# Kernel tuning notes

Measured on AMD Instinct MI355X. Metric: run time of the kernel, lower is better.

The kernel has to match this reference:

```python
import jax, jax.numpy as jnp
from jax import lax
import numpy as np

LENY = 1048576
NRBF = 11
A_PRIME = 1.0
B_PRIME = 1.0 / 60.0


def safe_sigmoid(x):
    return jax.nn.sigmoid(jnp.clip(x, -10.0, 10.0))


def setup_inputs() -> dict:
    key = jax.random.key(0)
    k = jax.random.split(key, 6)
    return {
        "yin": jax.random.normal(k[0], (LENY, 2), dtype=jnp.float32),
        "xstar_a": jax.random.normal(k[1], (LENY, 2), dtype=jnp.float32),
        "xstar_b": jax.random.normal(k[2], (LENY, 2), dtype=jnp.float32),
        "rbfw_raw": jax.random.normal(k[3], (1,), dtype=jnp.float32),
        "weights": jax.random.normal(k[4], (NRBF, 1), dtype=jnp.float32),
        "gain1_raw": jax.random.normal(k[5], (1,), dtype=jnp.float32),
        "gain2_raw": jax.random.normal(jax.random.fold_in(key, 7), (1,), dtype=jnp.float32),
    }


def reference(yin, xstar_a, xstar_b, rbfw_raw, weights, gain1_raw, gain2_raw):
    leny = yin.shape[0]
    # normalized time grid, zero-mean scaled to [-1, 1]
    t = jnp.linspace(0.0, leny - 1.0, leny, dtype=jnp.float32)
    t = t - t.mean()
    t = t / t.max()
    centers = jnp.linspace(t.min(), t.max(), NRBF, dtype=jnp.float32)  # (nRBF,)
    RBFw = safe_sigmoid(rbfw_raw)  # scalar-ish (1,)
    widths = RBFw * (t.max() - t.min()) / (NRBF - 1)
    # X_rbf is detached in the torch source (.detach().numpy()) -> stop_gradient
    X_rbf = lax.stop_gradient(
        jnp.exp(-((t[:, None] - centers[None, :]) ** 2) / (2.0 * widths ** 2))
    )  # (leny, nRBF)
    wt = safe_sigmoid(X_rbf @ weights)  # (leny, 1)

    gain1 = jnp.exp(gain1_raw)  # (1,)
    gain2 = jnp.exp(gain2_raw)  # (1,)

    # u depends only on observed yin, so it is fully vectorizable
    u1 = -gain1 * (yin - xstar_a)  # (leny, 2)
    u2 = -gain2 * (yin - xstar_b)  # (leny, 2)
    w = wt[:-1]  # (leny-1, 1)
    u_combined = u1[:-1] * (1.0 - w) + u2[:-1] * w  # (leny-1, 2)

    # affine linear recurrence: y[t+1] = A' y[t] + B' u[t], y[0] = yin[0]
    def step(carry, ut):
        nxt = A_PRIME * carry + B_PRIME * ut
        return nxt, nxt

    _, ys = lax.scan(step, yin[0], u_combined)  # (leny-1, 2)
    y = jnp.concatenate([yin[0:1], ys], axis=0)  # (leny, 2)
    return y, u_combined
```

## Files before the change

### kernel.cpp

```cpp
#include <hip/hip_runtime.h>

#define LENY  1048576
#define NU    (LENY - 1)
#define NRBF  11
#define NB    2048
#define NT    256
#define NW    (NT / 64)
#define PERT  2
#define CHUNK (NT * PERT)

typedef float v4f __attribute__((ext_vector_type(4)));

#define L2E 1.44269504088896340736f

__device__ __forceinline__ float fexp(float x) {
    return __builtin_amdgcn_exp2f(x * L2E);
}
__device__ __forceinline__ float sigmoid10(float x) {
    x = fminf(10.0f, fmaxf(-10.0f, x));
    const float e = __builtin_amdgcn_exp2f(-x * L2E);
    return __builtin_amdgcn_rcpf(1.0f + e);
}

__global__ __launch_bounds__(NT) void rbf_k1(
    const float2* __restrict__ yin,
    const float2* __restrict__ xa,
    const float2* __restrict__ xb,
    const float*  __restrict__ rbfw_raw,
    const float*  __restrict__ weights,
    const float*  __restrict__ g1raw,
    const float*  __restrict__ g2raw,
    float2* __restrict__ uout,
    double2* __restrict__ bsums)
{
    const int b = blockIdx.x, t = threadIdx.x;
    const int lane = t & 63, wid = t >> 6;
    const int base = b * CHUNK + t * PERT;

    const float RBFw    = sigmoid10(rbfw_raw[0]);
    const float wdt     = RBFw * 0.2f;
    const float negInvL = -L2E / (2.0f * wdt * wdt);
    const float g1 = fexp(g1raw[0]);
    const float g2 = fexp(g2raw[0]);
    const float Bf = (float)(1.0 / 60.0);

    float wj[NRBF];
    #pragma unroll
    for (int j = 0; j < NRBF; ++j) wj[j] = weights[j];

    const v4f yv = __builtin_nontemporal_load((const v4f*)yin + (base >> 1));
    const v4f av = __builtin_nontemporal_load((const v4f*)xa  + (base >> 1));
    const v4f bv = __builtin_nontemporal_load((const v4f*)xb  + (base >> 1));

    float ux[PERT], uy[PERT];
    double sx = 0.0, sy = 0.0;
    #pragma unroll
    for (int k = 0; k < PERT; ++k) {
        const int gi = base + k;
        const float ti = ((float)gi - 524287.5f) / 524287.5f;
        float dot = 0.0f;
        #pragma unroll
        for (int j = 0; j < NRBF; ++j) {
            const float c = -1.0f + 0.2f * (float)j;
            const float d = ti - c;
            dot += __builtin_amdgcn_exp2f(d * d * negInvL) * wj[j];
        }
        const float wt = sigmoid10(dot);
        const float eyx = yv[2*k], eyy = yv[2*k+1];
        const float eax = av[2*k], eay = av[2*k+1];
        const float ebx = bv[2*k], eby = bv[2*k+1];
        const float u1x = -g1 * (eyx - eax);
        const float u1y = -g1 * (eyy - eay);
        const float u2x = -g2 * (eyx - ebx);
        const float u2y = -g2 * (eyy - eby);
        ux[k] = u1x * (1.0f - wt) + u2x * wt;
        uy[k] = u1y * (1.0f - wt) + u2y * wt;
        sx += (double)(ux[k] * Bf);
        sy += (double)(uy[k] * Bf);
    }

    if (base + PERT <= NU) {
        v4f r = { ux[0], uy[0], ux[1], uy[1] };
        *((v4f*)uout + (base >> 1)) = r;
    } else {
        for (int k = 0; k < PERT; ++k)
            if (base + k < NU) uout[base + k] = make_float2(ux[k], uy[k]);
    }

    #pragma unroll
    for (int d = 32; d > 0; d >>= 1) {
        sx += __shfl_down(sx, d);
        sy += __shfl_down(sy, d);
    }
    __shared__ double2 wtot[NW];
    if (lane == 0) wtot[wid] = make_double2(sx, sy);
    __syncthreads();
    if (t == 0) {
        double tx = 0.0, ty = 0.0;
        #pragma unroll
        for (int w = 0; w < NW; ++w) { tx += wtot[w].x; ty += wtot[w].y; }
        bsums[b] = make_double2(tx, ty);
    }
}

__global__ __launch_bounds__(NT) void rbf_k2(
    const float2* __restrict__ yin,
    const float2* __restrict__ uin,
    const double2* __restrict__ bsums,
    float2* __restrict__ yout)
{
    const int b = blockIdx.x, t = threadIdx.x;
    const int lane = t & 63, wid = t >> 6;
    const int base = b * CHUNK + t * PERT;
    const float Bf = (float)(1.0 / 60.0);

    float u0x, u0y, u1x, u1y;
    if (base + PERT <= NU) {
        const v4f uv = *((const v4f*)uin + (base >> 1));
        u0x = uv[0]; u0y = uv[1]; u1x = uv[2]; u1y = uv[3];
    } else {
        const float2 z0 = (base < NU) ? uin[base] : make_float2(0.f, 0.f);
        u0x = z0.x; u0y = z0.y; u1x = 0.0f; u1y = 0.0f;
    }

    double ox = 0.0, oy = 0.0;
    for (int j = t; j < b; j += NT) { ox += bsums[j].x; oy += bsums[j].y; }
    #pragma unroll
    for (int d = 32; d > 0; d >>= 1) {
        ox += __shfl_down(ox, d);
        oy += __shfl_down(oy, d);
    }
    __shared__ double2 wred[NW];
    if (lane == 0) wred[wid] = make_double2(ox, oy);
    __syncthreads();
    double offx = 0.0, offy = 0.0;
    #pragma unroll
    for (int w = 0; w < NW; ++w) { offx += wred[w].x; offy += wred[w].y; }

    const double s0x = (double)(u0x * Bf), s0y = (double)(u0y * Bf);
    const double s1x = (double)(u1x * Bf), s1y = (double)(u1y * Bf);
    const double  sx = s0x + s1x, sy = s0y + s1y;
    double ix = sx, iy = sy;
    #pragma unroll
    for (int d = 1; d < 64; d <<= 1) {
        const double px = __shfl_up(ix, d, 64);
        const double py = __shfl_up(iy, d, 64);
        if (lane >= d) { ix += px; iy += py; }
    }
    __shared__ double2 wtot[NW];
    if (lane == 63) wtot[wid] = make_double2(ix, iy);
    __syncthreads();
    double wbx = 0.0, wby = 0.0;
    #pragma unroll
    for (int w = 0; w < NW; ++w)
        if (w < wid) { wbx += wtot[w].x; wby += wtot[w].y; }
    const double myex = wbx + ix - sx;
    const double myey = wby + iy - sy;

    const float2 y0 = yin[0];
    double runx = offx + myex, runy = offy + myey;
    const double y0x = (double)y0.x, y0y = (double)y0.y;

    const float o0x = (float)(y0x + runx);
    const float o0y = (float)(y0y + runy);
    runx += s0x; runy += s0y;
    const float o1x = (float)(y0x + runx);
    const float o1y = (float)(y0y + runy);
    v4f r = { o0x, o0y, o1x, o1y };
    __builtin_nontemporal_store(r, (v4f*)yout + (base >> 1));
}

extern "C" void kernel_launch(void* const* d_in, const int* in_sizes, int n_in,
                              void* d_out, int out_size, void* d_ws, size_t ws_size,
                              hipStream_t stream) {
    const float2* yin  = (const float2*)d_in[0];
    const float2* xa   = (const float2*)d_in[1];
    const float2* xb   = (const float2*)d_in[2];
    const float*  rbfw = (const float*)d_in[3];
    const float*  wts  = (const float*)d_in[4];
    const float*  g1   = (const float*)d_in[5];
    const float*  g2   = (const float*)d_in[6];

    float*  out  = (float*)d_out;
    float2* yout = (float2*)out;
    float2* uout = (float2*)(out + 2 * LENY);
    double2* bsums = (double2*)d_ws;

    rbf_k1<<<NB, NT, 0, stream>>>(yin, xa, xb, rbfw, wts, g1, g2, uout, bsums);
    rbf_k2<<<NB, NT, 0, stream>>>(yin, uout, bsums, yout);
}
```

Measured before the change: 18.99 us.

## Recompute u in second pass instead of writing and rereading it

The first kernel now only computes block sums of B*u without storing u. The second kernel reloads yin/xa/xb, recomputes u (including the RBF exponentials), writes u and y, and does the prefix scan. This removes the write of u in pass one and the read-back in pass two, but adds a second read of the three inputs plus duplicated transcendental work. Input loads become regular loads so they can stay in cache (about 24 MB fits in the MI355X's L2/Infinity Cache) for the second pass.

```diff
diff --git a/kernel.cpp b/kernel.cpp
--- a/kernel.cpp
+++ b/kernel.cpp
@@ -22,38 +22,13 @@
     return __builtin_amdgcn_rcpf(1.0f + e);
 }
 
-__global__ __launch_bounds__(NT) void rbf_k1(
-    const float2* __restrict__ yin,
-    const float2* __restrict__ xa,
-    const float2* __restrict__ xb,
-    const float*  __restrict__ rbfw_raw,
-    const float*  __restrict__ weights,
-    const float*  __restrict__ g1raw,
-    const float*  __restrict__ g2raw,
-    float2* __restrict__ uout,
-    double2* __restrict__ bsums)
+__device__ __forceinline__ void compute_u(
+    int base, const v4f yv, const v4f av, const v4f bv,
+    float negInvL, float g1, float g2, const float* wj,
+    float* ux, float* uy, double& sx, double& sy)
 {
-    const int b = blockIdx.x, t = threadIdx.x;
-    const int lane = t & 63, wid = t >> 6;
-    const int base = b * CHUNK + t * PERT;
-
-    const float RBFw    = sigmoid10(rbfw_raw[0]);
-    const float wdt     = RBFw * 0.2f;
-    const float negInvL = -L2E / (2.0f * wdt * wdt);
-    const float g1 = fexp(g1raw[0]);
-    const float g2 = fexp(g2raw[0]);
     const float Bf = (float)(1.0 / 60.0);
-
-    float wj[NRBF];
-    #pragma unroll
-    for (int j = 0; j < NRBF; ++j) wj[j] = weights[j];
-
-    const v4f yv = __builtin_nontemporal_load((const v4f*)yin + (base >> 1));
-    const v4f av = __builtin_nontemporal_load((const v4f*)xa  + (base >> 1));
-    const v4f bv = __builtin_nontemporal_load((const v4f*)xb  + (base >> 1));
-
-    float ux[PERT], uy[PERT];
-    double sx = 0.0, sy = 0.0;
+    sx = 0.0; sy = 0.0;
     #pragma unroll
     for (int k = 0; k < PERT; ++k) {
         const int gi = base + k;
@@ -78,14 +53,39 @@
         sx += (double)(ux[k] * Bf);
         sy += (double)(uy[k] * Bf);
     }
-
-    if (base + PERT <= NU) {
-        v4f r = { ux[0], uy[0], ux[1], uy[1] };
-        *((v4f*)uout + (base >> 1)) = r;
-    } else {
-        for (int k = 0; k < PERT; ++k)
-            if (base + k < NU) uout[base + k] = make_float2(ux[k], uy[k]);
-    }
+}
+
+__global__ __launch_bounds__(NT) void rbf_sum(
+    const float2* __restrict__ yin,
+    const float2* __restrict__ xa,
+    const float2* __restrict__ xb,
+    const float*  __restrict__ rbfw_raw,
+    const float*  __restrict__ weights,
+    const float*  __restrict__ g1raw,
+    const float*  __restrict__ g2raw,
+    double2* __restrict__ bsums)
+{
+    const int b = blockIdx.x, t = threadIdx.x;
+    const int lane = t & 63, wid = t >> 6;
+    const int base = b * CHUNK + t * PERT;
+
+    const float RBFw    = sigmoid10(rbfw_raw[0]);
+    const float wdt     = RBFw * 0.2f;
+    const float negInvL = -L2E / (2.0f * wdt * wdt);
+    const float g1 = fexp(g1raw[0]);
+    const float g2 = fexp(g2raw[0]);
+
+    float wj[NRBF];
+    #pragma unroll
+    for (int j = 0; j < NRBF; ++j) wj[j] = weights[j];
+
+    const v4f yv = *((const v4f*)yin + (base >> 1));
+    const v4f av = *((const v4f*)xa  + (base >> 1));
+    const v4f bv = *((const v4f*)xb  + (base >> 1));
+
+    float ux[PERT], uy[PERT];
+    double sx, sy;
+    compute_u(base, yv, av, bv, negInvL, g1, g2, wj, ux, uy, sx, sy);
 
     #pragma unroll
     for (int d = 32; d > 0; d >>= 1) {
@@ -103,10 +103,16 @@
     }
 }
 
-__global__ __launch_bounds__(NT) void rbf_k2(
+__global__ __launch_bounds__(NT) void rbf_out(
     const float2* __restrict__ yin,
-    const float2* __restrict__ uin,
+    const float2* __restrict__ xa,
+    const float2* __restrict__ xb,
+    const float*  __restrict__ rbfw_raw,
+    const float*  __restrict__ weights,
+    const float*  __restrict__ g1raw,
+    const float*  __restrict__ g2raw,
     const double2* __restrict__ bsums,
+    float2* __restrict__ uout,
     float2* __restrict__ yout)
 {
     const int b = blockIdx.x, t = threadIdx.x;
@@ -114,14 +120,20 @@
     const int base = b * CHUNK + t * PERT;
     const float Bf = (float)(1.0 / 60.0);
 
-    float u0x, u0y, u1x, u1y;
-    if (base + PERT <= NU) {
-        const v4f uv = *((const v4f*)uin + (base >> 1));
-        u0x = uv[0]; u0y = uv[1]; u1x = uv[2]; u1y = uv[3];
-    } else {
-        const float2 z0 = (base < NU) ? uin[base] : make_float2(0.f, 0.f);
-        u0x = z0.x; u0y = z0.y; u1x = 0.0f; u1y = 0.0f;
-    }
+    const float RBFw    = sigmoid10(rbfw_raw[0]);
+    const float wdt     = RBFw * 0.2f;
+    const float negInvL = -L2E / (2.0f * wdt * wdt);
+    const float g1 = fexp(g1raw[0]);
+    const float g2 = fexp(g2raw[0]);
+    const float2 y0 = yin[0];
+
+    float wj[NRBF];
+    #pragma unroll
+    for (int j = 0; j < NRBF; ++j) wj[j] = weights[j];
+
+    const v4f yv = *((const v4f*)yin + (base >> 1));
+    const v4f av = *((const v4f*)xa  + (base >> 1));
+    const v4f bv = *((const v4f*)xb  + (base >> 1));
 
     double ox = 0.0, oy = 0.0;
     for (int j = t; j < b; j += NT) { ox += bsums[j].x; oy += bsums[j].y; }
@@ -130,16 +142,11 @@
         ox += __shfl_down(ox, d);
         oy += __shfl_down(oy, d);
     }
-    __shared__ double2 wred[NW];
-    if (lane == 0) wred[wid] = make_double2(ox, oy);
-    __syncthreads();
-    double offx = 0.0, offy = 0.0;
-    #pragma unroll
-    for (int w = 0; w < NW; ++w) { offx += wred[w].x; offy += wred[w].y; }
-
-    const double s0x = (double)(u0x * Bf), s0y = (double)(u0y * Bf);
-    const double s1x = (double)(u1x * Bf), s1y = (double)(u1y * Bf);
-    const double  sx = s0x + s1x, sy = s0y + s1y;
+
+    float ux[PERT], uy[PERT];
+    double sx, sy;
+    compute_u(base, yv, av, bv, negInvL, g1, g2, wj, ux, uy, sx, sy);
+
     double ix = sx, iy = sy;
     #pragma unroll
     for (int d = 1; d < 64; d <<= 1) {
@@ -147,23 +154,37 @@
         const double py = __shfl_up(iy, d, 64);
         if (lane >= d) { ix += px; iy += py; }
     }
+
+    __shared__ double2 wred[NW];
     __shared__ double2 wtot[NW];
+    if (lane == 0)  wred[wid] = make_double2(ox, oy);
     if (lane == 63) wtot[wid] = make_double2(ix, iy);
     __syncthreads();
-    double wbx = 0.0, wby = 0.0;
-    #pragma unroll
-    for (int w = 0; w < NW; ++w)
+
+    double offx = 0.0, offy = 0.0, wbx = 0.0, wby = 0.0;
+    #pragma unroll
+    for (int w = 0; w < NW; ++w) {
+        offx += wred[w].x; offy += wred[w].y;
         if (w < wid) { wbx += wtot[w].x; wby += wtot[w].y; }
+    }
     const double myex = wbx + ix - sx;
     const double myey = wby + iy - sy;
 
-    const float2 y0 = yin[0];
+    if (base + PERT <= NU) {
+        v4f r = { ux[0], uy[0], ux[1], uy[1] };
+        __builtin_nontemporal_store(r, (v4f*)uout + (base >> 1));
+    } else {
+        for (int k = 0; k < PERT; ++k)
+            if (base + k < NU) uout[base + k] = make_float2(ux[k], uy[k]);
+    }
+
     double runx = offx + myex, runy = offy + myey;
     const double y0x = (double)y0.x, y0y = (double)y0.y;
 
     const float o0x = (float)(y0x + runx);
     const float o0y = (float)(y0y + runy);
-    runx += s0x; runy += s0y;
+    runx += (double)(ux[0] * Bf);
+    runy += (double)(uy[0] * Bf);
     const float o1x = (float)(y0x + runx);
     const float o1y = (float)(y0y + runy);
     v4f r = { o0x, o0y, o1x, o1y };
@@ -186,6 +207,7 @@
     float2* uout = (float2*)(out + 2 * LENY);
     double2* bsums = (double2*)d_ws;
 
-    rbf_k1<<<NB, NT, 0, stream>>>(yin, xa, xb, rbfw, wts, g1, g2, uout, bsums);
-    rbf_k2<<<NB, NT, 0, stream>>>(yin, uout, bsums, yout);
-}
+    rbf_sum<<<NB, NT, 0, stream>>>(yin, xa, xb, rbfw, wts, g1, g2, bsums);
+    rbf_out<<<NB, NT, 0, stream>>>(yin, xa, xb, rbfw, wts, g1, g2,
+                                   bsums, uout, yout);
+}
```

After: 19.20 us. About the same (+1.1%).

## Decouple kernel tiling, give k1 eight elements per thread and per-wave partial sums

Applied to the files above, without the earlier changes.

The first kernel now runs 512 blocks with eight elements per thread. Each wave writes its own partial sum straight to the workspace, so the shared-memory reduction and barrier are gone. Because 2048 wave sums map exactly onto the 2048 blocks of the second kernel, k2 keeps its indexing. In k2 the offset reduction and the intra-block scan now share a single barrier instead of two. The aim is to amortize the per-thread setup (weights, sigmoid and exp of the scalar parameters) and cut synchronization, at the cost of fewer concurrent blocks and the loss of nontemporal loads in k1.

```diff
diff --git a/kernel.cpp b/kernel.cpp
--- a/kernel.cpp
+++ b/kernel.cpp
@@ -3,11 +3,18 @@
 #define LENY  1048576
 #define NU    (LENY - 1)
 #define NRBF  11
-#define NB    2048
-#define NT    256
-#define NW    (NT / 64)
-#define PERT  2
-#define CHUNK (NT * PERT)
+
+#define NB1   512
+#define NT1   256
+#define PERT1 8
+#define CHUNK1 (NT1 * PERT1)
+
+#define NB2   2048
+#define NT2   256
+#define PERT2 2
+#define CHUNK2 (NT2 * PERT2)
+
+#define NW    4
 
 typedef float v4f __attribute__((ext_vector_type(4)));
 
@@ -22,7 +29,7 @@
     return __builtin_amdgcn_rcpf(1.0f + e);
 }
 
-__global__ __launch_bounds__(NT) void rbf_k1(
+__global__ __launch_bounds__(NT1) void rbf_k1(
     const float2* __restrict__ yin,
     const float2* __restrict__ xa,
     const float2* __restrict__ xb,
@@ -35,7 +42,7 @@
 {
     const int b = blockIdx.x, t = threadIdx.x;
     const int lane = t & 63, wid = t >> 6;
-    const int base = b * CHUNK + t * PERT;
+    const int base = b * CHUNK1 + t * PERT1;
 
     const float RBFw    = sigmoid10(rbfw_raw[0]);
     const float wdt     = RBFw * 0.2f;
@@ -48,14 +55,17 @@
     #pragma unroll
     for (int j = 0; j < NRBF; ++j) wj[j] = weights[j];
 
-    const v4f yv = __builtin_nontemporal_load((const v4f*)yin + (base >> 1));
-    const v4f av = __builtin_nontemporal_load((const v4f*)xa  + (base >> 1));
-    const v4f bv = __builtin_nontemporal_load((const v4f*)xb  + (base >> 1));
-
-    float ux[PERT], uy[PERT];
+    const v4f* yp = (const v4f*)yin + (base >> 1);
+    const v4f* ap = (const v4f*)xa  + (base >> 1);
+    const v4f* bp = (const v4f*)xb  + (base >> 1);
+    v4f yv[4], av[4], bv[4];
+    #pragma unroll
+    for (int q = 0; q < 4; ++q) { yv[q] = yp[q]; av[q] = ap[q]; bv[q] = bp[q]; }
+
+    float ux[PERT1], uy[PERT1];
     double sx = 0.0, sy = 0.0;
     #pragma unroll
-    for (int k = 0; k < PERT; ++k) {
+    for (int k = 0; k < PERT1; ++k) {
         const int gi = base + k;
         const float ti = ((float)gi - 524287.5f) / 524287.5f;
         float dot = 0.0f;
@@ -66,44 +76,46 @@
             dot += __builtin_amdgcn_exp2f(d * d * negInvL) * wj[j];
         }
         const float wt = sigmoid10(dot);
-        const float eyx = yv[2*k], eyy = yv[2*k+1];
-        const float eax = av[2*k], eay = av[2*k+1];
-        const float ebx = bv[2*k], eby = bv[2*k+1];
+        const float eyx = yv[k >> 1][(k & 1) * 2 + 0];
+        const float eyy = yv[k >> 1][(k & 1) * 2 + 1];
+        const float eax = av[k >> 1][(k & 1) * 2 + 0];
+        const float eay = av[k >> 1][(k & 1) * 2 + 1];
+        const float ebx = bv[k >> 1][(k & 1) * 2 + 0];
+        const float eby = bv[k >> 1][(k & 1) * 2 + 1];
         const float u1x = -g1 * (eyx - eax);
         const float u1y = -g1 * (eyy - eay);
         const float u2x = -g2 * (eyx - ebx);
         const float u2y = -g2 * (eyy - eby);
         ux[k] = u1x * (1.0f - wt) + u2x * wt;
         uy[k] = u1y * (1.0f - wt) + u2y * wt;
+    }
+
+    if (base + PERT1 <= NU) {
+        v4f* up = (v4f*)uout + (base >> 1);
+        #pragma unroll
+        for (int q = 0; q < 4; ++q) {
+            v4f r = { ux[2*q], uy[2*q], ux[2*q+1], uy[2*q+1] };
+            up[q] = r;
+        }
+    } else {
+        for (int k = 0; k < PERT1; ++k)
+            if (base + k < NU) uout[base + k] = make_float2(ux[k], uy[k]);
+    }
+
+    #pragma unroll
+    for (int k = 0; k < PERT1; ++k) {
         sx += (double)(ux[k] * Bf);
         sy += (double)(uy[k] * Bf);
     }
-
-    if (base + PERT <= NU) {
-        v4f r = { ux[0], uy[0], ux[1], uy[1] };
-        *((v4f*)uout + (base >> 1)) = r;
-    } else {
-        for (int k = 0; k < PERT; ++k)
-            if (base + k < NU) uout[base + k] = make_float2(ux[k], uy[k]);
-    }
-
     #pragma unroll
     for (int d = 32; d > 0; d >>= 1) {
         sx += __shfl_down(sx, d);
         sy += __shfl_down(sy, d);
     }
-    __shared__ double2 wtot[NW];
-    if (lane == 0) wtot[wid] = make_double2(sx, sy);
-    __syncthreads();
-    if (t == 0) {
-        double tx = 0.0, ty = 0.0;
-        #pragma unroll
-        for (int w = 0; w < NW; ++w) { tx += wtot[w].x; ty += wtot[w].y; }
-        bsums[b] = make_double2(tx, ty);
-    }
-}
-
-__global__ __launch_bounds__(NT) void rbf_k2(
+    if (lane == 0) bsums[b * NW + wid] = make_double2(sx, sy);
+}
+
+__global__ __launch_bounds__(NT2) void rbf_k2(
     const float2* __restrict__ yin,
     const float2* __restrict__ uin,
     const double2* __restrict__ bsums,
@@ -111,11 +123,11 @@
 {
     const int b = blockIdx.x, t = threadIdx.x;
     const int lane = t & 63, wid = t >> 6;
-    const int base = b * CHUNK + t * PERT;
+    const int base = b * CHUNK2 + t * PERT2;
     const float Bf = (float)(1.0 / 60.0);
 
     float u0x, u0y, u1x, u1y;
-    if (base + PERT <= NU) {
+    if (base + PERT2 <= NU) {
         const v4f uv = *((const v4f*)uin + (base >> 1));
         u0x = uv[0]; u0y = uv[1]; u1x = uv[2]; u1y = uv[3];
     } else {
@@ -124,18 +136,12 @@
     }
 
     double ox = 0.0, oy = 0.0;
-    for (int j = t; j < b; j += NT) { ox += bsums[j].x; oy += bsums[j].y; }
+    for (int j = t; j < b; j += NT2) { ox += bsums[j].x; oy += bsums[j].y; }
     #pragma unroll
     for (int d = 32; d > 0; d >>= 1) {
         ox += __shfl_down(ox, d);
         oy += __shfl_down(oy, d);
     }
-    __shared__ double2 wred[NW];
-    if (lane == 0) wred[wid] = make_double2(ox, oy);
-    __syncthreads();
-    double offx = 0.0, offy = 0.0;
-    #pragma unroll
-    for (int w = 0; w < NW; ++w) { offx += wred[w].x; offy += wred[w].y; }
 
     const double s0x = (double)(u0x * Bf), s0y = (double)(u0y * Bf);
     const double s1x = (double)(u1x * Bf), s1y = (double)(u1y * Bf);
@@ -147,13 +153,19 @@
         const double py = __shfl_up(iy, d, 64);
         if (lane >= d) { ix += px; iy += py; }
     }
+
+    __shared__ double2 wred[NW];
     __shared__ double2 wtot[NW];
+    if (lane == 0)  wred[wid] = make_double2(ox, oy);
     if (lane == 63) wtot[wid] = make_double2(ix, iy);
     __syncthreads();
-    double wbx = 0.0, wby = 0.0;
-    #pragma unroll
-    for (int w = 0; w < NW; ++w)
+
+    double offx = 0.0, offy = 0.0, wbx = 0.0, wby = 0.0;
+    #pragma unroll
+    for (int w = 0; w < NW; ++w) {
+        offx += wred[w].x; offy += wred[w].y;
         if (w < wid) { wbx += wtot[w].x; wby += wtot[w].y; }
+    }
     const double myex = wbx + ix - sx;
     const double myey = wby + iy - sy;
 
@@ -186,6 +198,6 @@
     float2* uout = (float2*)(out + 2 * LENY);
     double2* bsums = (double2*)d_ws;
 
-    rbf_k1<<<NB, NT, 0, stream>>>(yin, xa, xb, rbfw, wts, g1, g2, uout, bsums);
-    rbf_k2<<<NB, NT, 0, stream>>>(yin, uout, bsums, yout);
-}
+    rbf_k1<<<NB1, NT1, 0, stream>>>(yin, xa, xb, rbfw, wts, g1, g2, uout, bsums);
+    rbf_k2<<<NB2, NT2, 0, stream>>>(yin, uout, bsums, yout);
+}
```

After: 22.92 us. 20.7% more time.
